# Kernel tuning notes

Hardware: AMD Instinct MI355X
Metric: run time of the kernel (lower is better)

The kernel has to match this reference:

```python
import jax, jax.numpy as jnp
import numpy as np

EPS = 1e-5

def conv2d(x, w, b=None, pad=1):
    # x: [B,C,H,W], w: [O,I,kh,kw]
    y = jax.lax.conv_general_dilated(x, w, (1, 1), [(pad, pad), (pad, pad)],
                                     dimension_numbers=('NCHW', 'OIHW', 'NCHW'))
    if b is not None:
        y = y + b[None, :, None, None]
    return y

def bn(x, g, b, m, v):
    # inference-mode batchnorm
    inv = g / jnp.sqrt(v + EPS)
    return x * inv[None, :, None, None] + (b - m * inv)[None, :, None, None]

def coord_conv(x, w, b):
    B, C, H, W = x.shape
    yy = jnp.broadcast_to(jnp.linspace(-1.0, 1.0, H)[:, None], (H, W))
    xx = jnp.broadcast_to(jnp.linspace(-1.0, 1.0, W)[None, :], (H, W))
    coords = jnp.broadcast_to(jnp.stack([xx, yy])[None], (B, 2, H, W)).astype(x.dtype)
    return conv2d(jnp.concatenate([x, coords], axis=1), w, b, pad=1)

def deform_conv(x, offset, w):
    # deformable conv v1, 3x3, pad=1, stride=1, no bias
    B, C, H, W = x.shape
    K = 9
    # offset channels interleaved (y, x) per kernel tap
    off = offset.reshape(B, K, 2, H, W)
    off_y, off_x = off[:, :, 0], off[:, :, 1]          # [B,9,H,W]
    k = jnp.arange(K)
    ko_y = (k // 3 - 1).astype(x.dtype)[None, :, None, None]
    ko_x = (k % 3 - 1).astype(x.dtype)[None, :, None, None]
    base_y = jnp.arange(H, dtype=x.dtype)[None, None, :, None]
    base_x = jnp.arange(W, dtype=x.dtype)[None, None, None, :]
    py = base_y + ko_y + off_y                          # [B,9,H,W]
    px = base_x + ko_x + off_x
    xf = x.reshape(B, C, H * W)
    y0 = jnp.floor(py)
    x0 = jnp.floor(px)
    acc = jnp.zeros((B, C, K, H, W), x.dtype)
    for dy in (0.0, 1.0):
        for dx in (0.0, 1.0):
            yy = y0 + dy
            xx = x0 + dx
            wgt = (1.0 - jnp.abs(py - yy)) * (1.0 - jnp.abs(px - xx))
            valid = (yy >= 0) & (yy < H) & (xx >= 0) & (xx < W)
            wgt = jnp.where(valid, wgt, 0.0)            # zero padding OOB
            yi = jnp.clip(yy, 0, H - 1).astype(jnp.int32)
            xi = jnp.clip(xx, 0, W - 1).astype(jnp.int32)
            idx = (yi * W + xi).reshape(B, K * H * W)
            v = jnp.take_along_axis(xf, idx[:, None, :], axis=2).reshape(B, C, K, H, W)
            acc = acc + v * wgt[:, None]
    wk = w.reshape(w.shape[0], w.shape[1], K)           # [O,I,9]
    return jnp.einsum('bckhw,ock->bohw', acc, wk)

def setup_inputs() -> dict:
    key = jax.random.key(0)
    ks = jax.random.split(key, 16)
    d_model, hd = 256, 64
    B, H, W = 8, 96, 96
    f32 = jnp.float32
    def bn_params(k):
        k1, k2, k3 = jax.random.split(k, 3)
        return (1.0 + 0.1 * jax.random.normal(k1, (hd,), f32),
                0.1 * jax.random.normal(k2, (hd,), f32),
                0.1 * jax.random.normal(k3, (hd,), f32),
                0.5 + jax.random.uniform(jax.random.fold_in(k, 7), (hd,), f32))
    bn1 = bn_params(ks[1]); bn2 = bn_params(ks[2]); bn3 = bn_params(ks[3]); bn4 = bn_params(ks[4])
    inp = {
        'features': jax.random.normal(ks[0], (B, H, W, d_model), f32),
        'coord_w': 0.05 * jax.random.normal(ks[5], (hd, d_model + 2, 3, 3), f32),
        'coord_b': jnp.zeros((hd,), f32),
        'bn1_g': bn1[0], 'bn1_b': bn1[1], 'bn1_m': bn1[2], 'bn1_v': bn1[3],
        'off_w': 0.01 * jax.random.normal(ks[6], (18, hd, 3, 3), f32),
        'off_b': 0.01 * jax.random.normal(ks[7], (18,), f32),
        'dc_w': 0.05 * jax.random.normal(ks[8], (hd, hd, 3, 3), f32),
        'bn2_g': bn2[0], 'bn2_b': bn2[1], 'bn2_m': bn2[2], 'bn2_v': bn2[3],
        'r1_w': 0.05 * jax.random.normal(ks[9], (hd, hd, 3, 3), f32),
        'bn3_g': bn3[0], 'bn3_b': bn3[1], 'bn3_m': bn3[2], 'bn3_v': bn3[3],
        'r2_w': 0.05 * jax.random.normal(ks[10], (hd, hd, 3, 3), f32),
        'bn4_g': bn4[0], 'bn4_b': bn4[1], 'bn4_m': bn4[2], 'bn4_v': bn4[3],
        'out_w': 0.1 * jax.random.normal(ks[11], (1, hd, 1, 1), f32),
        'out_b': jnp.zeros((1,), f32),
    }
    return inp

def reference(features, coord_w, coord_b, bn1_g, bn1_b, bn1_m, bn1_v,
              off_w, off_b, dc_w, bn2_g, bn2_b, bn2_m, bn2_v,
              r1_w, bn3_g, bn3_b, bn3_m, bn3_v,
              r2_w, bn4_g, bn4_b, bn4_m, bn4_v, out_w, out_b):
    x = jnp.transpose(features, (0, 3, 1, 2))           # NHWC -> NCHW
    x = jax.nn.relu(bn(coord_conv(x, coord_w, coord_b), bn1_g, bn1_b, bn1_m, bn1_v))
    offset = conv2d(x, off_w, off_b, pad=1)
    x = deform_conv(x, offset, dc_w)
    x = jax.nn.relu(bn(x, bn2_g, bn2_b, bn2_m, bn2_v))
    x = jax.nn.relu(bn(conv2d(x, r1_w, None, pad=1), bn3_g, bn3_b, bn3_m, bn3_v))
    x = jax.nn.relu(bn(conv2d(x, r2_w, None, pad=1), bn4_g, bn4_b, bn4_m, bn4_v))
    return jax.nn.sigmoid(conv2d(x, out_w, out_b, pad=0))
```

## Files before the change

kernel.cpp:

```cpp
#include <hip/hip_runtime.h>


typedef unsigned short u16;
typedef unsigned int u32;
typedef __attribute__((ext_vector_type(8)))  short bf16x8;
typedef __attribute__((ext_vector_type(16))) float f32x16;

#define EPSBN 1e-5f

__device__ __forceinline__ u16 f2bf(float f) {
  u32 u = __builtin_bit_cast(u32, f);
  u32 r = u + 0x7FFFu + ((u >> 16) & 1u);
  return (u16)(r >> 16);
}
__device__ __forceinline__ u32 pk2(float a, float b) {
  return (u32)f2bf(a) | ((u32)f2bf(b) << 16);
}
__device__ __forceinline__ float lo2f(u32 w) { return __builtin_bit_cast(float, w << 16); }
__device__ __forceinline__ float hi2f(u32 w) { return __builtin_bit_cast(float, w & 0xFFFF0000u); }

#define N_WCF 147456
#define N_WCC 9216
#define N_WOF 18432
#define N_W64 36864
#define N_ALLW (N_WCF + N_WCC + N_WOF + 3*N_W64)

__global__ __launch_bounds__(256) void prep_kernel(
    const float* __restrict__ coord_w, const float* __restrict__ off_w,
    const float* __restrict__ dc_w, const float* __restrict__ r1_w,
    const float* __restrict__ r2_w,
    u16* __restrict__ wcf, u16* __restrict__ wcc, u16* __restrict__ wof,
    u16* __restrict__ wdf, u16* __restrict__ wr1, u16* __restrict__ wr2)
{
  int i = blockIdx.x * 256 + threadIdx.x;
  if (i >= N_ALLW) return;
  int d = i;
  if (d < N_WCF) {
    int j = d & 7, lane = (d >> 3) & 63, frag = d >> 9;
    int nt = frag & 1, h = (frag >> 1) & 3, tap = (frag >> 3) % 9, cc = (frag >> 3) / 9;
    int ic = cc * 64 + h * 16 + ((lane >> 5) << 3) + j;
    int oc = nt * 32 + (lane & 31);
    wcf[d] = f2bf(coord_w[((size_t)oc * 258 + ic) * 9 + tap]);
    return;
  }
  d -= N_WCF;
  if (d < N_WCC) {
    int j = d & 7, lane = (d >> 3) & 63, frag = d >> 9;
    int nt = frag & 1, tap = frag >> 1;
    int ic = 256 + ((lane >> 5) << 3) + j;
    int oc = nt * 32 + (lane & 31);
    wcc[d] = (ic < 258) ? f2bf(coord_w[((size_t)oc * 258 + ic) * 9 + tap]) : (u16)0;
    return;
  }
  d -= N_WCC;
  if (d < N_WOF) {
    int j = d & 7, lane = (d >> 3) & 63, frag = d >> 9;
    int h = frag & 3, tap = frag >> 2;
    int ic = h * 16 + ((lane >> 5) << 3) + j;
    int oc = lane & 31;
    wof[d] = (oc < 18) ? f2bf(off_w[((size_t)oc * 64 + ic) * 9 + tap]) : (u16)0;
    return;
  }
  d -= N_WOF;
  int seg = d / N_W64;
  int e = d - seg * N_W64;
  int j = e & 7, lane = (e >> 3) & 63, frag = e >> 9;
  int nt = frag & 1, h = (frag >> 1) & 3, tap = frag >> 3;
  int ic = h * 16 + ((lane >> 5) << 3) + j;
  int oc = nt * 32 + (lane & 31);
  const float* src = (seg == 0) ? dc_w : (seg == 1) ? r1_w : r2_w;
  u16* dst = (seg == 0) ? wdf : (seg == 1) ? wr1 : wr2;
  dst[e] = f2bf(src[((size_t)oc * 64 + ic) * 9 + tap]);
}

__global__ __launch_bounds__(512, 2) void coord_conv_kernel(
    const float* __restrict__ feat, const u16* __restrict__ wcf,
    const u16* __restrict__ wcc, const float* __restrict__ cb,
    const float* __restrict__ g, const float* __restrict__ bb,
    const float* __restrict__ m, const float* __restrict__ v,
    u16* __restrict__ x1b)
{
  __shared__ __align__(16) u16 tile[6 * 34 * 72];
  const int t = threadIdx.x;
  const int wv = t >> 6, lane = t & 63;
  const int l31 = lane & 31, l5 = lane >> 5;
  const int rp = wv & 1, ntw = (wv >> 1) & 1, kh = wv >> 2;
  const int x0 = blockIdx.x * 32, y0 = blockIdx.y * 4, b = blockIdx.z;

  f32x16 acc[2] = {};
  float4 pa[4], pb[4];
  bf16x8 wfr[18];

  auto issueF = [&](int cc) {
    #pragma unroll
    for (int r = 0; r < 4; ++r) {
      const int i = t + r * 512;
      const float4 z = {0.f, 0.f, 0.f, 0.f};
      pa[r] = z; pb[r] = z;
      if (i < 1632) {
        const int px = i >> 3, gg = i & 7;
        const int ly = px / 34, lx = px - ly * 34;
        const int gy = y0 + ly - 1, gx = x0 + lx - 1;
        if ((unsigned)gy < 96u && (unsigned)gx < 96u) {
          const float* p = feat + ((size_t)((b * 96 + gy) * 96 + gx)) * 256
                           + cc * 64 + gg * 8;
          pa[r] = *(const float4*)p;
          pb[r] = *(const float4*)(p + 4);
        }
      }
    }
  };
  auto commitF = [&]() {
    #pragma unroll
    for (int r = 0; r < 4; ++r) {
      const int i = t + r * 512;
      if (i < 1632) {
        const int px = i >> 3, gg = i & 7;
        uint4 o;
        o.x = pk2(pa[r].x, pa[r].y); o.y = pk2(pa[r].z, pa[r].w);
        o.z = pk2(pb[r].x, pb[r].y); o.w = pk2(pb[r].z, pb[r].w);
        *(uint4*)(tile + px * 72 + gg * 8) = o;
      }
    }
  };
  auto loadW = [&](int cc) {
    #pragma unroll
    for (int tap = 0; tap < 9; ++tap)
      #pragma unroll
      for (int hh = 0; hh < 2; ++hh) {
        const int h = kh * 2 + hh;
        wfr[tap * 2 + hh] = *(const bf16x8*)(wcf +
            ((size_t)((((cc * 9 + tap) * 4 + h) * 2) + ntw)) * 512 + lane * 8);
      }
  };

  issueF(0);
  loadW(0);
  for (int cc = 0; cc < 4; ++cc) {
    __syncthreads();
    commitF();
    __syncthreads();
    if (cc < 3) issueF(cc + 1);
    #pragma unroll
    for (int tap = 0; tap < 9; ++tap) {
      const int dy = tap / 3, dx = tap - dy * 3;
      #pragma unroll
      for (int hh = 0; hh < 2; ++hh) {
        const bf16x8 bfr = wfr[tap * 2 + hh];
        #pragma unroll
        for (int ai = 0; ai < 2; ++ai) {
          const bf16x8 afr = *(const bf16x8*)(tile +
              ((rp * 2 + ai + dy) * 34 + l31 + dx) * 72
              + (kh * 2 + hh) * 16 + l5 * 8);
          acc[ai] = __builtin_amdgcn_mfma_f32_32x32x16_bf16(afr, bfr, acc[ai],
                                                            0, 0, 0);
        }
      }
    }
    if (cc < 3) loadW(cc + 1);
  }

  bf16x8 wcr[9];
  if (kh == 0) {
    #pragma unroll
    for (int tap = 0; tap < 9; ++tap)
      wcr[tap] = *(const bf16x8*)(wcc + ((size_t)(tap * 2 + ntw)) * 512
                                  + lane * 8);
  }
  __syncthreads();
  for (int i = t; i < 408; i += 512) {
    const int px = i >> 1, gg = i & 1;
    const int ly = px / 34, lx = px - ly * 34;
    const int gy = y0 + ly - 1, gx = x0 + lx - 1;
    uint4 o = {0u, 0u, 0u, 0u};
    if (gg == 0 && (unsigned)gy < 96u && (unsigned)gx < 96u) {
      const float xx = -1.f + (2.f / 95.f) * (float)gx;
      const float yy = -1.f + (2.f / 95.f) * (float)gy;
      o.x = pk2(xx, yy);
    }
    *(uint4*)(tile + (ly * 34 + lx) * 72 + gg * 8) = o;
  }
  __syncthreads();
  if (kh == 0) {
    #pragma unroll
    for (int tap = 0; tap < 9; ++tap) {
      const int dy = tap / 3, dx = tap - dy * 3;
      #pragma unroll
      for (int ai = 0; ai < 2; ++ai) {
        const bf16x8 afr = *(const bf16x8*)(tile +
            ((rp * 2 + ai + dy) * 34 + l31 + dx) * 72 + l5 * 8);
        acc[ai] = __builtin_amdgcn_mfma_f32_32x32x16_bf16(afr, wcr[tap],
                                                          acc[ai], 0, 0, 0);
      }
    }
  }

  float* redk = (float*)tile;
  const int slot = wv & 3;
  #pragma unroll
  for (int ai = 0; ai < 2; ++ai) {
    __syncthreads();
    if (kh == 1) {
      #pragma unroll
      for (int r = 0; r < 16; ++r)
        redk[(r * 4 + slot) * 64 + lane] = acc[ai][r];
    }
    __syncthreads();
    if (kh == 0) {
      #pragma unroll
      for (int r = 0; r < 16; ++r)
        acc[ai][r] += redk[(r * 4 + slot) * 64 + lane];
    }
  }

  if (kh == 0) {
    const int oc = ntw * 32 + l31;
    const float inv = g[oc] * rsqrtf(v[oc] + EPSBN);
    const float sh = bb[oc] - m[oc] * inv + cb[oc] * inv;
    #pragma unroll
    for (int ai = 0; ai < 2; ++ai) {
      const int y = y0 + rp * 2 + ai;
      #pragma unroll
      for (int r = 0; r < 16; ++r) {
        const int xr = (r & 3) + 8 * (r >> 2) + 4 * l5;
        const float val = fmaxf(fmaf(acc[ai][r], inv, sh), 0.f);
        x1b[((size_t)((b * 96 + y) * 96 + x0 + xr)) * 64 + oc] = f2bf(val);
      }
    }
  }
}

template<int NN, int EPI>
__global__ __launch_bounds__(512, 2) void conv64_kernel(
    const u16* __restrict__ xin, const u16* __restrict__ wf,
    const float* __restrict__ bias,
    const float* __restrict__ g, const float* __restrict__ bb,
    const float* __restrict__ m, const float* __restrict__ v,
    const float* __restrict__ ow, const float* __restrict__ ob,
    void* __restrict__ outp)
{
  __shared__ __align__(16) u16 tile[6 * 34 * 72];
  __shared__ float red2[2][128];
  const int t = threadIdx.x;
  const int wv = t >> 6, lane = t & 63;
  const int l31 = lane & 31, l5 = lane >> 5;
  const int rp  = (NN == 2) ? (wv & 1) : 0;
  const int ntw = (NN == 2) ? ((wv >> 1) & 1) : 0;
  const int row = (NN == 2) ? 0 : (wv & 3);
  const int kh  = wv >> 2;
  const int x0 = blockIdx.x * 32, y0 = blockIdx.y * 4, b = blockIdx.z;

  uint4 pf[4];
  #pragma unroll
  for (int r = 0; r < 4; ++r) {
    const int i = t + r * 512;
    const uint4 z = {0u, 0u, 0u, 0u};
    pf[r] = z;
    if (i < 1632) {
      const int px = i >> 3, gg = i & 7;
      const int ly = px / 34, lx = px - ly * 34;
      const int gy = y0 + ly - 1, gx = x0 + lx - 1;
      if ((unsigned)gy < 96u && (unsigned)gx < 96u)
        pf[r] = *(const uint4*)(xin + (((size_t)((b * 96 + gy) * 96 + gx)) << 6)
                                + gg * 8);
    }
  }
  bf16x8 wfr[18];
  #pragma unroll
  for (int tap = 0; tap < 9; ++tap)
    #pragma unroll
    for (int hh = 0; hh < 2; ++hh) {
      const int h = kh * 2 + hh;
      const size_t f = (NN == 2) ? (size_t)((tap * 4 + h) * 2 + ntw)
                                 : (size_t)(tap * 4 + h);
      wfr[tap * 2 + hh] = *(const bf16x8*)(wf + f * 512 + lane * 8);
    }
  #pragma unroll
  for (int r = 0; r < 4; ++r) {
    const int i = t + r * 512;
    if (i < 1632) {
      const int px = i >> 3, gg = i & 7;
      *(uint4*)(tile + px * 72 + gg * 8) = pf[r];
    }
  }
  __syncthreads();

  constexpr int NA = (NN == 2) ? 2 : 1;
  f32x16 acc[NA] = {};
  #pragma unroll
  for (int tap = 0; tap < 9; ++tap) {
    const int dy = tap / 3, dx = tap - dy * 3;
    #pragma unroll
    for (int hh = 0; hh < 2; ++hh) {
      const int h = kh * 2 + hh;
      #pragma unroll
      for (int ai = 0; ai < NA; ++ai) {
        const int rr = (NN == 2) ? (rp * 2 + ai) : row;
        const bf16x8 afr = *(const bf16x8*)(tile +
            ((rr + dy) * 34 + l31 + dx) * 72 + h * 16 + l5 * 8);
        acc[ai] = __builtin_amdgcn_mfma_f32_32x32x16_bf16(afr, wfr[tap * 2 + hh],
                                                          acc[ai], 0, 0, 0);
      }
    }
  }

  float* redk = (float*)tile;
  const int slot = (NN == 2) ? (wv & 3) : row;
  #pragma unroll
  for (int ai = 0; ai < NA; ++ai) {
    __syncthreads();
    if (kh == 1) {
      #pragma unroll
      for (int r = 0; r < 16; ++r)
        redk[(r * 4 + slot) * 64 + lane] = acc[ai][r];
    }
    __syncthreads();
    if (kh == 0) {
      #pragma unroll
      for (int r = 0; r < 16; ++r)
        acc[ai][r] += redk[(r * 4 + slot) * 64 + lane];
    }
  }

  if constexpr (EPI == 0) {
    if (kh == 0) {
      u16* xo = (u16*)outp;
      const int oc = ntw * 32 + l31;
      const float inv = g[oc] * rsqrtf(v[oc] + EPSBN);
      const float sh = bb[oc] - m[oc] * inv;
      #pragma unroll
      for (int ai = 0; ai < NA; ++ai) {
        const int y = y0 + rp * 2 + ai;
        #pragma unroll
        for (int r = 0; r < 16; ++r) {
          const int xr = (r & 3) + 8 * (r >> 2) + 4 * l5;
          const float val = fmaxf(fmaf(acc[ai][r], inv, sh), 0.f);
          xo[((size_t)((b * 96 + y) * 96 + x0 + xr)) * 64 + oc] = f2bf(val);
        }
      }
    }
  } else if constexpr (EPI == 1) {
    if (kh == 0 && l31 < 18) {
      float* fo = (float*)outp;
      const int y = y0 + row;
      const float bs = bias[l31];
      #pragma unroll
      for (int r = 0; r < 16; ++r) {
        const int xr = (r & 3) + 8 * (r >> 2) + 4 * l5;
        fo[((size_t)((b * 96 + y) * 96 + x0 + xr)) * 18 + l31] = acc[0][r] + bs;
      }
    }
  } else {
    if (kh == 0) {
      const int oc = ntw * 32 + l31;
      const float inv = g[oc] * rsqrtf(v[oc] + EPSBN);
      const float sh = bb[oc] - m[oc] * inv;
      const float wo = ow[oc];
      #pragma unroll
      for (int ai = 0; ai < NA; ++ai) {
        float pr[16];
        #pragma unroll
        for (int r = 0; r < 16; ++r) {
          const float val = fmaxf(fmaf(acc[ai][r], inv, sh), 0.f);
          pr[r] = val * wo;
        }
        #pragma unroll
        for (int mask = 1; mask <= 16; mask <<= 1)
          #pragma unroll
          for (int r = 0; r < 16; ++r)
            pr[r] += __shfl_xor(pr[r], mask);
        if (l31 == 0) {
          #pragma unroll
          for (int r = 0; r < 16; ++r) {
            const int xr = (r & 3) + 8 * (r >> 2) + 4 * l5;
            red2[ntw][(rp * 2 + ai) * 32 + xr] = pr[r];
          }
        }
      }
    }
    __syncthreads();
    if (t < 128) {
      float* fo = (float*)outp;
      const int yy = y0 + (t >> 5), xx = x0 + (t & 31);
      const float val = red2[0][t] + red2[1][t] + ob[0];
      fo[(size_t)(b * 96 + yy) * 96 + xx] = 1.f / (1.f + expf(-val));
    }
  }
}

__global__ __launch_bounds__(512, 4) void deform_kernel(
    const u16* __restrict__ x1b, const float* __restrict__ off,
    const u16* __restrict__ wdf,
    const float* __restrict__ g, const float* __restrict__ bb,
    const float* __restrict__ m, const float* __restrict__ v,
    u16* __restrict__ x2b)
{
  __shared__ __align__(16) u16 s[2 * 128 * 72];
  __shared__ float offs[128 * 18];
  const int t = threadIdx.x;
  const int wv = t >> 6, lane = t & 63;
  const int l31 = lane & 31, l5 = lane >> 5;
  const int mt = wv & 3, ntw = wv >> 2;
  const int x0 = blockIdx.x * 16, y0 = blockIdx.y * 8, b = blockIdx.z;

  {
    float po[5];
    #pragma unroll
    for (int r = 0; r < 5; ++r) {
      const int i = t + r * 512;
      po[r] = 0.f;
      if (i < 2304) {
        const int p = i / 18, c = i - p * 18;
        const int gy = y0 + (p >> 4), gx = x0 + (p & 15);
        po[r] = off[((size_t)((b * 96 + gy) * 96 + gx)) * 18 + c];
      }
    }
    #pragma unroll
    for (int r = 0; r < 5; ++r) {
      const int i = t + r * 512;
      if (i < 2304) offs[i] = po[r];
    }
  }
  __syncthreads();

  const int sp = t >> 2, part = t & 3;
  const int sy = y0 + (sp >> 4), sx = x0 + (sp & 15);

  uint4 gbuf[8];
  float w4[4];

  auto prefetch = [&](int k) {
    const float oy = offs[sp * 18 + 2 * k];
    const float ox = offs[sp * 18 + 2 * k + 1];
    const float py = (float)(sy + k / 3 - 1) + oy;
    const float px = (float)(sx + k % 3 - 1) + ox;
    const float yf = floorf(py), xf = floorf(px);
    const float fy = py - yf, fx = px - xf;
    const int yi = (int)yf, xi = (int)xf;
    #pragma unroll
    for (int cor = 0; cor < 4; ++cor) {
      const int cy = yi + (cor >> 1), cx = xi + (cor & 1);
      const uint4 z = {0u, 0u, 0u, 0u};
      gbuf[2 * cor] = z; gbuf[2 * cor + 1] = z;
      const float wy = (cor & 2) ? fy : 1.f - fy;
      const float wx = (cor & 1) ? fx : 1.f - fx;
      w4[cor] = 0.f;
      if ((unsigned)cy < 96u && (unsigned)cx < 96u) {
        w4[cor] = wy * wx;
        const u16* p = x1b + ((size_t)((b * 96 + cy) * 96 + cx)) * 64
                       + part * 16;
        gbuf[2 * cor]     = *(const uint4*)p;
        gbuf[2 * cor + 1] = *(const uint4*)(p + 8);
      }
    }
  };
  auto combine = [&](u16* dst) {
    float val[16];
    #pragma unroll
    for (int j = 0; j < 16; ++j) val[j] = 0.f;
    #pragma unroll
    for (int cor = 0; cor < 4; ++cor) {
      const float wgt = w4[cor];
      const u32 uu[8] = {gbuf[2 * cor].x, gbuf[2 * cor].y,
                         gbuf[2 * cor].z, gbuf[2 * cor].w,
                         gbuf[2 * cor + 1].x, gbuf[2 * cor + 1].y,
                         gbuf[2 * cor + 1].z, gbuf[2 * cor + 1].w};
      #pragma unroll
      for (int u = 0; u < 8; ++u) {
        val[2 * u]     = fmaf(wgt, lo2f(uu[u]), val[2 * u]);
        val[2 * u + 1] = fmaf(wgt, hi2f(uu[u]), val[2 * u + 1]);
      }
    }
    u32 pk[8];
    #pragma unroll
    for (int u = 0; u < 8; ++u) pk[u] = pk2(val[2 * u], val[2 * u + 1]);
    uint4 w0 = {pk[0], pk[1], pk[2], pk[3]};
    uint4 w1 = {pk[4], pk[5], pk[6], pk[7]};
    *(uint4*)(dst + sp * 72 + part * 16) = w0;
    *(uint4*)(dst + sp * 72 + part * 16 + 8) = w1;
  };

  f32x16 acc = {};

  prefetch(0);
  combine(s);
  __syncthreads();

  for (int k = 0; k < 9; ++k) {
    u16* cur = s + (k & 1) * 9216;
    if (k < 8) prefetch(k + 1);
    #pragma unroll
    for (int h = 0; h < 4; ++h) {
      const bf16x8 afr = *(const bf16x8*)(cur + (mt * 32 + l31) * 72
                                          + h * 16 + l5 * 8);
      const bf16x8 bfr = *(const bf16x8*)(wdf +
          ((size_t)((k * 4 + h) * 2 + ntw)) * 512 + lane * 8);
      acc = __builtin_amdgcn_mfma_f32_32x32x16_bf16(afr, bfr, acc, 0, 0, 0);
    }
    if (k < 8) combine(s + ((k + 1) & 1) * 9216);
    __syncthreads();
  }

  const int oc = ntw * 32 + l31;
  const float inv = g[oc] * rsqrtf(v[oc] + EPSBN);
  const float sh = bb[oc] - m[oc] * inv;
  #pragma unroll
  for (int r = 0; r < 16; ++r) {
    const int pxi = mt * 32 + (r & 3) + 8 * (r >> 2) + 4 * l5;
    const int y = y0 + (pxi >> 4), x = x0 + (pxi & 15);
    const float val = fmaxf(fmaf(acc[r], inv, sh), 0.f);
    x2b[((size_t)((b * 96 + y) * 96 + x)) * 64 + oc] = f2bf(val);
  }
}

extern "C" void kernel_launch(void* const* d_in, const int* in_sizes, int n_in,
                              void* d_out, int out_size, void* d_ws,
                              size_t ws_size, hipStream_t stream)
{
  (void)in_sizes; (void)n_in; (void)out_size; (void)ws_size;
  const float* features = (const float*)d_in[0];
  const float* coord_w  = (const float*)d_in[1];
  const float* coord_b  = (const float*)d_in[2];
  const float* bn1g = (const float*)d_in[3];
  const float* bn1b = (const float*)d_in[4];
  const float* bn1m = (const float*)d_in[5];
  const float* bn1v = (const float*)d_in[6];
  const float* off_w = (const float*)d_in[7];
  const float* off_b = (const float*)d_in[8];
  const float* dc_w  = (const float*)d_in[9];
  const float* bn2g = (const float*)d_in[10];
  const float* bn2b = (const float*)d_in[11];
  const float* bn2m = (const float*)d_in[12];
  const float* bn2v = (const float*)d_in[13];
  const float* r1_w = (const float*)d_in[14];
  const float* bn3g = (const float*)d_in[15];
  const float* bn3b = (const float*)d_in[16];
  const float* bn3m = (const float*)d_in[17];
  const float* bn3v = (const float*)d_in[18];
  const float* r2_w = (const float*)d_in[19];
  const float* bn4g = (const float*)d_in[20];
  const float* bn4b = (const float*)d_in[21];
  const float* bn4m = (const float*)d_in[22];
  const float* bn4v = (const float*)d_in[23];
  const float* out_w = (const float*)d_in[24];
  const float* out_b = (const float*)d_in[25];

  char* W = (char*)d_ws;
  float* offb = (float*)W;
  u16*   x1b  = (u16*)(W + 5308416);
  u16*   x2b  = (u16*)(W + 14745600);
  u16*   x3b  = (u16*)(W + 24182784);
  u16*   wcf  = (u16*)(W + 33619968);
  u16*   wcc  = wcf + N_WCF;
  u16*   wof  = wcc + N_WCC;
  u16*   wdf  = wof + N_WOF;
  u16*   wr1  = wdf + N_W64;
  u16*   wr2  = wr1 + N_W64;

  prep_kernel<<<(N_ALLW + 255) / 256, 256, 0, stream>>>(
      coord_w, off_w, dc_w, r1_w, r2_w, wcf, wcc, wof, wdf, wr1, wr2);

  dim3 grid(3, 24, 8);
  dim3 gridD(6, 12, 8);

  coord_conv_kernel<<<grid, 512, 0, stream>>>(
      features, wcf, wcc, coord_b, bn1g, bn1b, bn1m, bn1v, x1b);
  conv64_kernel<1, 1><<<grid, 512, 0, stream>>>(
      x1b, wof, off_b, nullptr, nullptr, nullptr, nullptr, nullptr, nullptr,
      (void*)offb);
  deform_kernel<<<gridD, 512, 0, stream>>>(
      x1b, offb, wdf, bn2g, bn2b, bn2m, bn2v, x2b);
  conv64_kernel<2, 0><<<grid, 512, 0, stream>>>(
      x2b, wr1, nullptr, bn3g, bn3b, bn3m, bn3v, nullptr, nullptr, (void*)x3b);
  conv64_kernel<2, 2><<<grid, 512, 0, stream>>>(
      x3b, wr2, nullptr, bn4g, bn4b, bn4m, bn4v, out_w, out_b, d_out);
}
```

Before: 251.0 us.

## Pre-convert features to bf16 and stage conv tiles via direct global-to-LDS loads

The prep kernel now also converts the NHWC fp32 feature map to bf16 and zeroes a small pad buffer. The conv kernels stage input halos with global_load_lds 16-byte copies, redirecting out-of-bounds pixels to the zero buffer instead of loading through registers. Blocks shrink to 256 threads (4 waves), each wave computing both 32-channel output tiles, with weights read directly from global memory per MFMA rather than preloaded into registers. Coordinate channels get their own small LDS tile. This adds an extra full pass over the features in prep and drops the register-level prefetch overlap in coord_conv.

```diff
diff --git a/kernel.cpp b/kernel.cpp
--- a/kernel.cpp
+++ b/kernel.cpp
@@ -18,6 +18,12 @@
 }
 __device__ __forceinline__ float lo2f(u32 w) { return __builtin_bit_cast(float, w << 16); }
 __device__ __forceinline__ float hi2f(u32 w) { return __builtin_bit_cast(float, w & 0xFFFF0000u); }
+
+__device__ __forceinline__ void gload_lds16(const void* g, void* l) {
+  __builtin_amdgcn_global_load_lds(
+      (const __attribute__((address_space(1))) unsigned int*)g,
+      (__attribute__((address_space(3))) unsigned int*)l, 16, 0, 0);
+}
 
 #define N_WCF 147456
 #define N_WCC 9216
@@ -25,14 +31,32 @@
 #define N_W64 36864
 #define N_ALLW (N_WCF + N_WCC + N_WOF + 3*N_W64)
 
+#define FBK_BLOCKS 9216
+#define WT_BLOCKS  1116
+
 __global__ __launch_bounds__(256) void prep_kernel(
+    const float* __restrict__ feat,
     const float* __restrict__ coord_w, const float* __restrict__ off_w,
     const float* __restrict__ dc_w, const float* __restrict__ r1_w,
     const float* __restrict__ r2_w,
+    u16* __restrict__ fb,
     u16* __restrict__ wcf, u16* __restrict__ wcc, u16* __restrict__ wof,
-    u16* __restrict__ wdf, u16* __restrict__ wr1, u16* __restrict__ wr2)
+    u16* __restrict__ wdf, u16* __restrict__ wr1, u16* __restrict__ wr2,
+    u32* __restrict__ zb)
 {
-  int i = blockIdx.x * 256 + threadIdx.x;
+  const int t = threadIdx.x;
+  if (blockIdx.x < FBK_BLOCKS) {
+    const int e = (blockIdx.x * 256 + t) * 8;
+    const float4 f0 = *(const float4*)(feat + e);
+    const float4 f1 = *(const float4*)(feat + e + 4);
+    uint4 o;
+    o.x = pk2(f0.x, f0.y); o.y = pk2(f0.z, f0.w);
+    o.z = pk2(f1.x, f1.y); o.w = pk2(f1.z, f1.w);
+    *(uint4*)(fb + e) = o;
+    return;
+  }
+  int i = (blockIdx.x - FBK_BLOCKS) * 256 + t;
+  if (i < 64) zb[i] = 0u;
   if (i >= N_ALLW) return;
   int d = i;
   if (d < N_WCF) {
@@ -73,296 +97,262 @@
   dst[e] = f2bf(src[((size_t)oc * 64 + ic) * 9 + tap]);
 }
 
-__global__ __launch_bounds__(512, 2) void coord_conv_kernel(
-    const float* __restrict__ feat, const u16* __restrict__ wcf,
+__device__ __forceinline__ u32 stage_desc(int slot, int x0, int y0, int b,
+                                          int px_stride) {
+  const int px = slot / 9, part = slot - px * 9;
+  if (part >= 8 || px >= 204) return 0xFFFFFFFFu;
+  const int ly = px / 34, lx = px - ly * 34;
+  const int gy = y0 + ly - 1, gx = x0 + lx - 1;
+  if ((unsigned)gy >= 96u || (unsigned)gx >= 96u) return 0xFFFFFFFFu;
+  return (u32)(((b * 96 + gy) * 96 + gx) * px_stride + part * 16);
+}
+
+__global__ __launch_bounds__(256, 4) void coord_conv_kernel(
+    const u16* __restrict__ fb, const u16* __restrict__ wcf,
     const u16* __restrict__ wcc, const float* __restrict__ cb,
     const float* __restrict__ g, const float* __restrict__ bb,
     const float* __restrict__ m, const float* __restrict__ v,
-    u16* __restrict__ x1b)
+    u16* __restrict__ x1b, const u32* __restrict__ zb)
 {
-  __shared__ __align__(16) u16 tile[6 * 34 * 72];
+  __shared__ __align__(16) u16 tile[16384];
+  __shared__ __align__(16) u16 ct[204 * 16];
   const int t = threadIdx.x;
   const int wv = t >> 6, lane = t & 63;
   const int l31 = lane & 31, l5 = lane >> 5;
-  const int rp = wv & 1, ntw = (wv >> 1) & 1, kh = wv >> 2;
+  const int rp = wv & 1, kh = wv >> 1;
   const int x0 = blockIdx.x * 32, y0 = blockIdx.y * 4, b = blockIdx.z;
 
-  f32x16 acc[2] = {};
-  float4 pa[4], pb[4];
-  bf16x8 wfr[18];
-
-  auto issueF = [&](int cc) {
-    #pragma unroll
-    for (int r = 0; r < 4; ++r) {
-      const int i = t + r * 512;
-      const float4 z = {0.f, 0.f, 0.f, 0.f};
-      pa[r] = z; pb[r] = z;
-      if (i < 1632) {
-        const int px = i >> 3, gg = i & 7;
-        const int ly = px / 34, lx = px - ly * 34;
-        const int gy = y0 + ly - 1, gx = x0 + lx - 1;
-        if ((unsigned)gy < 96u && (unsigned)gx < 96u) {
-          const float* p = feat + ((size_t)((b * 96 + gy) * 96 + gx)) * 256
-                           + cc * 64 + gg * 8;
-          pa[r] = *(const float4*)p;
-          pb[r] = *(const float4*)(p + 4);
-        }
-      }
-    }
-  };
-  auto commitF = [&]() {
-    #pragma unroll
-    for (int r = 0; r < 4; ++r) {
-      const int i = t + r * 512;
-      if (i < 1632) {
-        const int px = i >> 3, gg = i & 7;
-        uint4 o;
-        o.x = pk2(pa[r].x, pa[r].y); o.y = pk2(pa[r].z, pa[r].w);
-        o.z = pk2(pb[r].x, pb[r].y); o.w = pk2(pb[r].z, pb[r].w);
-        *(uint4*)(tile + px * 72 + gg * 8) = o;
-      }
-    }
-  };
-  auto loadW = [&](int cc) {
-    #pragma unroll
-    for (int tap = 0; tap < 9; ++tap)
+  u32 desc[8];
+  #pragma unroll
+  for (int k = 0; k < 8; ++k)
+    desc[k] = stage_desc((wv + 4 * k) * 64 + lane, x0, y0, b, 512);
+
+  if (t < 204) {
+    const int ly = t / 34, lx = t - ly * 34;
+    const int gy = y0 + ly - 1, gx = x0 + lx - 1;
+    uint4 o0 = {0u, 0u, 0u, 0u}, o1 = {0u, 0u, 0u, 0u};
+    if ((unsigned)gy < 96u && (unsigned)gx < 96u) {
+      const float xx = -1.f + (2.f / 95.f) * (float)gx;
+      const float yy = -1.f + (2.f / 95.f) * (float)gy;
+      o0.x = pk2(xx, yy);
+    }
+    *(uint4*)(ct + t * 16) = o0;
+    *(uint4*)(ct + t * 16 + 8) = o1;
+  }
+
+  f32x16 acc[2][2] = {};
+
+  for (int cc = 0; cc < 4; ++cc) {
+    #pragma unroll
+    for (int k = 0; k < 8; ++k) {
+      const char* src = (desc[k] == 0xFFFFFFFFu)
+          ? (const char*)zb : (const char*)fb + desc[k] + cc * 128;
+      gload_lds16(src, (char*)tile + (wv + 4 * k) * 1024);
+    }
+    __syncthreads();
+    #pragma unroll
+    for (int tap = 0; tap < 9; ++tap) {
+      const int dy = tap / 3, dx = tap - dy * 3;
       #pragma unroll
       for (int hh = 0; hh < 2; ++hh) {
         const int h = kh * 2 + hh;
-        wfr[tap * 2 + hh] = *(const bf16x8*)(wcf +
-            ((size_t)((((cc * 9 + tap) * 4 + h) * 2) + ntw)) * 512 + lane * 8);
-      }
-  };
-
-  issueF(0);
-  loadW(0);
-  for (int cc = 0; cc < 4; ++cc) {
+        const bf16x8 a0 = *(const bf16x8*)(tile +
+            ((rp * 2 + 0 + dy) * 34 + l31 + dx) * 72 + h * 16 + l5 * 8);
+        const bf16x8 a1 = *(const bf16x8*)(tile +
+            ((rp * 2 + 1 + dy) * 34 + l31 + dx) * 72 + h * 16 + l5 * 8);
+        #pragma unroll
+        for (int nt = 0; nt < 2; ++nt) {
+          const bf16x8 bfr = *(const bf16x8*)(wcf +
+              ((size_t)((((cc * 9 + tap) * 4 + h) * 2) + nt)) * 512 + lane * 8);
+          acc[0][nt] = __builtin_amdgcn_mfma_f32_32x32x16_bf16(a0, bfr,
+                                                               acc[0][nt], 0, 0, 0);
+          acc[1][nt] = __builtin_amdgcn_mfma_f32_32x32x16_bf16(a1, bfr,
+                                                               acc[1][nt], 0, 0, 0);
+        }
+      }
+    }
     __syncthreads();
-    commitF();
-    __syncthreads();
-    if (cc < 3) issueF(cc + 1);
+  }
+
+  if (kh == 0) {
     #pragma unroll
     for (int tap = 0; tap < 9; ++tap) {
       const int dy = tap / 3, dx = tap - dy * 3;
-      #pragma unroll
-      for (int hh = 0; hh < 2; ++hh) {
-        const bf16x8 bfr = wfr[tap * 2 + hh];
-        #pragma unroll
-        for (int ai = 0; ai < 2; ++ai) {
-          const bf16x8 afr = *(const bf16x8*)(tile +
-              ((rp * 2 + ai + dy) * 34 + l31 + dx) * 72
-              + (kh * 2 + hh) * 16 + l5 * 8);
-          acc[ai] = __builtin_amdgcn_mfma_f32_32x32x16_bf16(afr, bfr, acc[ai],
-                                                            0, 0, 0);
+      const bf16x8 a0 = *(const bf16x8*)(ct +
+          ((rp * 2 + 0 + dy) * 34 + l31 + dx) * 16 + l5 * 8);
+      const bf16x8 a1 = *(const bf16x8*)(ct +
+          ((rp * 2 + 1 + dy) * 34 + l31 + dx) * 16 + l5 * 8);
+      #pragma unroll
+      for (int nt = 0; nt < 2; ++nt) {
+        const bf16x8 bfr = *(const bf16x8*)(wcc +
+            ((size_t)(tap * 2 + nt)) * 512 + lane * 8);
+        acc[0][nt] = __builtin_amdgcn_mfma_f32_32x32x16_bf16(a0, bfr,
+                                                             acc[0][nt], 0, 0, 0);
+        acc[1][nt] = __builtin_amdgcn_mfma_f32_32x32x16_bf16(a1, bfr,
+                                                             acc[1][nt], 0, 0, 0);
+      }
+    }
+  }
+
+  float* redk = (float*)tile;
+  __syncthreads();
+  if (kh == 1) {
+    #pragma unroll
+    for (int ai = 0; ai < 2; ++ai)
+      #pragma unroll
+      for (int nt = 0; nt < 2; ++nt)
+        #pragma unroll
+        for (int r = 0; r < 16; ++r)
+          redk[(((rp * 2 + ai) * 2 + nt) * 16 + r) * 64 + lane] = acc[ai][nt][r];
+  }
+  __syncthreads();
+  if (kh == 0) {
+    #pragma unroll
+    for (int ai = 0; ai < 2; ++ai)
+      #pragma unroll
+      for (int nt = 0; nt < 2; ++nt) {
+        #pragma unroll
+        for (int r = 0; r < 16; ++r)
+          acc[ai][nt][r] += redk[(((rp * 2 + ai) * 2 + nt) * 16 + r) * 64 + lane];
+        const int oc = nt * 32 + l31;
+        const float inv = g[oc] * rsqrtf(v[oc] + EPSBN);
+        const float sh = bb[oc] - m[oc] * inv + cb[oc] * inv;
+        const int y = y0 + rp * 2 + ai;
+        #pragma unroll
+        for (int r = 0; r < 16; ++r) {
+          const int xr = (r & 3) + 8 * (r >> 2) + 4 * l5;
+          const float val = fmaxf(fmaf(acc[ai][nt][r], inv, sh), 0.f);
+          x1b[((size_t)((b * 96 + y) * 96 + x0 + xr)) * 64 + oc] = f2bf(val);
         }
       }
-    }
-    if (cc < 3) loadW(cc + 1);
-  }
-
-  bf16x8 wcr[9];
-  if (kh == 0) {
-    #pragma unroll
-    for (int tap = 0; tap < 9; ++tap)
-      wcr[tap] = *(const bf16x8*)(wcc + ((size_t)(tap * 2 + ntw)) * 512
-                                  + lane * 8);
-  }
-  __syncthreads();
-  for (int i = t; i < 408; i += 512) {
-    const int px = i >> 1, gg = i & 1;
-    const int ly = px / 34, lx = px - ly * 34;
-    const int gy = y0 + ly - 1, gx = x0 + lx - 1;
-    uint4 o = {0u, 0u, 0u, 0u};
-    if (gg == 0 && (unsigned)gy < 96u && (unsigned)gx < 96u) {
-      const float xx = -1.f + (2.f / 95.f) * (float)gx;
-      const float yy = -1.f + (2.f / 95.f) * (float)gy;
-      o.x = pk2(xx, yy);
-    }
-    *(uint4*)(tile + (ly * 34 + lx) * 72 + gg * 8) = o;
-  }
-  __syncthreads();
-  if (kh == 0) {
-    #pragma unroll
-    for (int tap = 0; tap < 9; ++tap) {
-      const int dy = tap / 3, dx = tap - dy * 3;
-      #pragma unroll
-      for (int ai = 0; ai < 2; ++ai) {
-        const bf16x8 afr = *(const bf16x8*)(tile +
-            ((rp * 2 + ai + dy) * 34 + l31 + dx) * 72 + l5 * 8);
-        acc[ai] = __builtin_amdgcn_mfma_f32_32x32x16_bf16(afr, wcr[tap],
-                                                          acc[ai], 0, 0, 0);
-      }
-    }
-  }
-
-  float* redk = (float*)tile;
-  const int slot = wv & 3;
-  #pragma unroll
-  for (int ai = 0; ai < 2; ++ai) {
-    __syncthreads();
-    if (kh == 1) {
-      #pragma unroll
-      for (int r = 0; r < 16; ++r)
-        redk[(r * 4 + slot) * 64 + lane] = acc[ai][r];
-    }
-    __syncthreads();
-    if (kh == 0) {
-      #pragma unroll
-      for (int r = 0; r < 16; ++r)
-        acc[ai][r] += redk[(r * 4 + slot) * 64 + lane];
-    }
-  }
-
-  if (kh == 0) {
-    const int oc = ntw * 32 + l31;
-    const float inv = g[oc] * rsqrtf(v[oc] + EPSBN);
-    const float sh = bb[oc] - m[oc] * inv + cb[oc] * inv;
-    #pragma unroll
-    for (int ai = 0; ai < 2; ++ai) {
-      const int y = y0 + rp * 2 + ai;
-      #pragma unroll
-      for (int r = 0; r < 16; ++r) {
-        const int xr = (r & 3) + 8 * (r >> 2) + 4 * l5;
-        const float val = fmaxf(fmaf(acc[ai][r], inv, sh), 0.f);
-        x1b[((size_t)((b * 96 + y) * 96 + x0 + xr)) * 64 + oc] = f2bf(val);
-      }
-    }
   }
 }
 
 template<int NN, int EPI>
-__global__ __launch_bounds__(512, 2) void conv64_kernel(
+__global__ __launch_bounds__(256, 4) void conv64_kernel(
     const u16* __restrict__ xin, const u16* __restrict__ wf,
     const float* __restrict__ bias,
     const float* __restrict__ g, const float* __restrict__ bb,
     const float* __restrict__ m, const float* __restrict__ v,
     const float* __restrict__ ow, const float* __restrict__ ob,
-    void* __restrict__ outp)
+    void* __restrict__ outp, const u32* __restrict__ zb)
 {
-  __shared__ __align__(16) u16 tile[6 * 34 * 72];
-  __shared__ float red2[2][128];
+  __shared__ __align__(16) u16 tile[16384];
+  __shared__ float red2[128];
   const int t = threadIdx.x;
   const int wv = t >> 6, lane = t & 63;
   const int l31 = lane & 31, l5 = lane >> 5;
-  const int rp  = (NN == 2) ? (wv & 1) : 0;
-  const int ntw = (NN == 2) ? ((wv >> 1) & 1) : 0;
-  const int row = (NN == 2) ? 0 : (wv & 3);
-  const int kh  = wv >> 2;
+  const int rp = wv & 1, kh = wv >> 1;
   const int x0 = blockIdx.x * 32, y0 = blockIdx.y * 4, b = blockIdx.z;
 
-  uint4 pf[4];
   #pragma unroll
-  for (int r = 0; r < 4; ++r) {
-    const int i = t + r * 512;
-    const uint4 z = {0u, 0u, 0u, 0u};
-    pf[r] = z;
-    if (i < 1632) {
-      const int px = i >> 3, gg = i & 7;
-      const int ly = px / 34, lx = px - ly * 34;
-      const int gy = y0 + ly - 1, gx = x0 + lx - 1;
-      if ((unsigned)gy < 96u && (unsigned)gx < 96u)
-        pf[r] = *(const uint4*)(xin + (((size_t)((b * 96 + gy) * 96 + gx)) << 6)
-                                + gg * 8);
-    }
-  }
-  bf16x8 wfr[18];
-  #pragma unroll
-  for (int tap = 0; tap < 9; ++tap)
-    #pragma unroll
-    for (int hh = 0; hh < 2; ++hh) {
-      const int h = kh * 2 + hh;
-      const size_t f = (NN == 2) ? (size_t)((tap * 4 + h) * 2 + ntw)
-                                 : (size_t)(tap * 4 + h);
-      wfr[tap * 2 + hh] = *(const bf16x8*)(wf + f * 512 + lane * 8);
-    }
-  #pragma unroll
-  for (int r = 0; r < 4; ++r) {
-    const int i = t + r * 512;
-    if (i < 1632) {
-      const int px = i >> 3, gg = i & 7;
-      *(uint4*)(tile + px * 72 + gg * 8) = pf[r];
-    }
-  }
-  __syncthreads();
-
-  constexpr int NA = (NN == 2) ? 2 : 1;
-  f32x16 acc[NA] = {};
+  for (int k = 0; k < 8; ++k) {
+    const u32 d = stage_desc((wv + 4 * k) * 64 + lane, x0, y0, b, 128);
+    const char* src = (d == 0xFFFFFFFFu) ? (const char*)zb
+                                         : (const char*)xin + d;
+    gload_lds16(src, (char*)tile + (wv + 4 * k) * 1024);
+  }
+  __syncthreads();
+
+  f32x16 acc[2][NN] = {};
   #pragma unroll
   for (int tap = 0; tap < 9; ++tap) {
     const int dy = tap / 3, dx = tap - dy * 3;
     #pragma unroll
     for (int hh = 0; hh < 2; ++hh) {
       const int h = kh * 2 + hh;
-      #pragma unroll
-      for (int ai = 0; ai < NA; ++ai) {
-        const int rr = (NN == 2) ? (rp * 2 + ai) : row;
-        const bf16x8 afr = *(const bf16x8*)(tile +
-            ((rr + dy) * 34 + l31 + dx) * 72 + h * 16 + l5 * 8);
-        acc[ai] = __builtin_amdgcn_mfma_f32_32x32x16_bf16(afr, wfr[tap * 2 + hh],
-                                                          acc[ai], 0, 0, 0);
+      const bf16x8 a0 = *(const bf16x8*)(tile +
+          ((rp * 2 + 0 + dy) * 34 + l31 + dx) * 72 + h * 16 + l5 * 8);
+      const bf16x8 a1 = *(const bf16x8*)(tile +
+          ((rp * 2 + 1 + dy) * 34 + l31 + dx) * 72 + h * 16 + l5 * 8);
+      #pragma unroll
+      for (int nt = 0; nt < NN; ++nt) {
+        const size_t f = (NN == 2) ? (size_t)((tap * 4 + h) * 2 + nt)
+                                   : (size_t)(tap * 4 + h);
+        const bf16x8 bfr = *(const bf16x8*)(wf + f * 512 + lane * 8);
+        acc[0][nt] = __builtin_amdgcn_mfma_f32_32x32x16_bf16(a0, bfr,
+                                                             acc[0][nt], 0, 0, 0);
+        acc[1][nt] = __builtin_amdgcn_mfma_f32_32x32x16_bf16(a1, bfr,
+                                                             acc[1][nt], 0, 0, 0);
       }
     }
   }
 
   float* redk = (float*)tile;
-  const int slot = (NN == 2) ? (wv & 3) : row;
-  #pragma unroll
-  for (int ai = 0; ai < NA; ++ai) {
-    __syncthreads();
-    if (kh == 1) {
-      #pragma unroll
-      for (int r = 0; r < 16; ++r)
-        redk[(r * 4 + slot) * 64 + lane] = acc[ai][r];
-    }
-    __syncthreads();
-    if (kh == 0) {
-      #pragma unroll
-      for (int r = 0; r < 16; ++r)
-        acc[ai][r] += redk[(r * 4 + slot) * 64 + lane];
-    }
-  }
+  __syncthreads();
+  if (kh == 1) {
+    #pragma unroll
+    for (int ai = 0; ai < 2; ++ai)
+      #pragma unroll
+      for (int nt = 0; nt < NN; ++nt)
+        #pragma unroll
+        for (int r = 0; r < 16; ++r)
+          redk[(((rp * 2 + ai) * NN + nt) * 16 + r) * 64 + lane] = acc[ai][nt][r];
+  }
+  __syncthreads();
 
   if constexpr (EPI == 0) {
     if (kh == 0) {
       u16* xo = (u16*)outp;
-      const int oc = ntw * 32 + l31;
-      const float inv = g[oc] * rsqrtf(v[oc] + EPSBN);
-      const float sh = bb[oc] - m[oc] * inv;
-      #pragma unroll
-      for (int ai = 0; ai < NA; ++ai) {
-        const int y = y0 + rp * 2 + ai;
-        #pragma unroll
-        for (int r = 0; r < 16; ++r) {
-          const int xr = (r & 3) + 8 * (r >> 2) + 4 * l5;
-          const float val = fmaxf(fmaf(acc[ai][r], inv, sh), 0.f);
-          xo[((size_t)((b * 96 + y) * 96 + x0 + xr)) * 64 + oc] = f2bf(val);
+      #pragma unroll
+      for (int ai = 0; ai < 2; ++ai)
+        #pragma unroll
+        for (int nt = 0; nt < NN; ++nt) {
+          #pragma unroll
+          for (int r = 0; r < 16; ++r)
+            acc[ai][nt][r] += redk[(((rp * 2 + ai) * NN + nt) * 16 + r) * 64 + lane];
+          const int oc = nt * 32 + l31;
+          const float inv = g[oc] * rsqrtf(v[oc] + EPSBN);
+          const float sh = bb[oc] - m[oc] * inv;
+          const int y = y0 + rp * 2 + ai;
+          #pragma unroll
+          for (int r = 0; r < 16; ++r) {
+            const int xr = (r & 3) + 8 * (r >> 2) + 4 * l5;
+            const float val = fmaxf(fmaf(acc[ai][nt][r], inv, sh), 0.f);
+            xo[((size_t)((b * 96 + y) * 96 + x0 + xr)) * 64 + oc] = f2bf(val);
+          }
         }
-      }
     }
   } else if constexpr (EPI == 1) {
-    if (kh == 0 && l31 < 18) {
+    if (kh == 0) {
       float* fo = (float*)outp;
-      const int y = y0 + row;
-      const float bs = bias[l31];
-      #pragma unroll
-      for (int r = 0; r < 16; ++r) {
-        const int xr = (r & 3) + 8 * (r >> 2) + 4 * l5;
-        fo[((size_t)((b * 96 + y) * 96 + x0 + xr)) * 18 + l31] = acc[0][r] + bs;
+      #pragma unroll
+      for (int ai = 0; ai < 2; ++ai) {
+        #pragma unroll
+        for (int r = 0; r < 16; ++r)
+          acc[ai][0][r] += redk[(((rp * 2 + ai) * NN + 0) * 16 + r) * 64 + lane];
+        if (l31 < 18) {
+          const float bs = bias[l31];
+          const int y = y0 + rp * 2 + ai;
+          #pragma unroll
+          for (int r = 0; r < 16; ++r) {
+            const int xr = (r & 3) + 8 * (r >> 2) + 4 * l5;
+            fo[((size_t)((b * 96 + y) * 96 + x0 + xr)) * 18 + l31] =
+                acc[ai][0][r] + bs;
+          }
+        }
       }
     }
   } else {
     if (kh == 0) {
-      const int oc = ntw * 32 + l31;
-      const float inv = g[oc] * rsqrtf(v[oc] + EPSBN);
-      const float sh = bb[oc] - m[oc] * inv;
-      const float wo = ow[oc];
-      #pragma unroll
-      for (int ai = 0; ai < NA; ++ai) {
+      #pragma unroll
+      for (int ai = 0; ai < 2; ++ai) {
         float pr[16];
         #pragma unroll
-        for (int r = 0; r < 16; ++r) {
-          const float val = fmaxf(fmaf(acc[ai][r], inv, sh), 0.f);
-          pr[r] = val * wo;
+        for (int r = 0; r < 16; ++r) pr[r] = 0.f;
+        #pragma unroll
+        for (int nt = 0; nt < NN; ++nt) {
+          const int oc = nt * 32 + l31;
+          const float inv = g[oc] * rsqrtf(v[oc] + EPSBN);
+          const float sh = bb[oc] - m[oc] * inv;
+          const float wo = ow[oc];
+          #pragma unroll
+          for (int r = 0; r < 16; ++r) {
+            const float a = acc[ai][nt][r] +
+                redk[(((rp * 2 + ai) * NN + nt) * 16 + r) * 64 + lane];
+            const float val = fmaxf(fmaf(a, inv, sh), 0.f);
+            pr[r] = fmaf(val, wo, pr[r]);
+          }
         }
         #pragma unroll
         for (int mask = 1; mask <= 16; mask <<= 1)
@@ -373,7 +363,7 @@
           #pragma unroll
           for (int r = 0; r < 16; ++r) {
             const int xr = (r & 3) + 8 * (r >> 2) + 4 * l5;
-            red2[ntw][(rp * 2 + ai) * 32 + xr] = pr[r];
+            red2[(rp * 2 + ai) * 32 + xr] = pr[r];
           }
         }
       }
@@ -382,7 +372,7 @@
     if (t < 128) {
       float* fo = (float*)outp;
       const int yy = y0 + (t >> 5), xx = x0 + (t & 31);
-      const float val = red2[0][t] + red2[1][t] + ob[0];
+      const float val = red2[t] + ob[0];
       fo[(size_t)(b * 96 + yy) * 96 + xx] = 1.f / (1.f + expf(-val));
     }
   }
@@ -556,22 +546,26 @@
   u16*   wdf  = wof + N_WOF;
   u16*   wr1  = wdf + N_W64;
   u16*   wr2  = wr1 + N_W64;
-
-  prep_kernel<<<(N_ALLW + 255) / 256, 256, 0, stream>>>(
-      coord_w, off_w, dc_w, r1_w, r2_w, wcf, wcc, wof, wdf, wr1, wr2);
+  u16*   fb   = (u16*)(W + 34191360);
+  u32*   zb   = (u32*)(W + 71940096);
+
+  prep_kernel<<<FBK_BLOCKS + WT_BLOCKS, 256, 0, stream>>>(
+      features, coord_w, off_w, dc_w, r1_w, r2_w,
+      fb, wcf, wcc, wof, wdf, wr1, wr2, zb);
 
   dim3 grid(3, 24, 8);
   dim3 gridD(6, 12, 8);
 
-  coord_conv_kernel<<<grid, 512, 0, stream>>>(
-      features, wcf, wcc, coord_b, bn1g, bn1b, bn1m, bn1v, x1b);
-  conv64_kernel<1, 1><<<grid, 512, 0, stream>>>(
+  coord_conv_kernel<<<grid, 256, 0, stream>>>(
+      fb, wcf, wcc, coord_b, bn1g, bn1b, bn1m, bn1v, x1b, zb);
+  conv64_kernel<1, 1><<<grid, 256, 0, stream>>>(
       x1b, wof, off_b, nullptr, nullptr, nullptr, nullptr, nullptr, nullptr,
-      (void*)offb);
+      (void*)offb, zb);
   deform_kernel<<<gridD, 512, 0, stream>>>(
       x1b, offb, wdf, bn2g, bn2b, bn2m, bn2v, x2b);
-  conv64_kernel<2, 0><<<grid, 512, 0, stream>>>(
-      x2b, wr1, nullptr, bn3g, bn3b, bn3m, bn3v, nullptr, nullptr, (void*)x3b);
-  conv64_kernel<2, 2><<<grid, 512, 0, stream>>>(
-      x3b, wr2, nullptr, bn4g, bn4b, bn4m, bn4v, out_w, out_b, d_out);
-}
+  conv64_kernel<2, 0><<<grid, 256, 0, stream>>>(
+      x2b, wr1, nullptr, bn3g, bn3b, bn3m, bn3v, nullptr, nullptr,
+      (void*)x3b, zb);
+  conv64_kernel<2, 2><<<grid, 256, 0, stream>>>(
+      x3b, wr2, nullptr, bn4g, bn4b, bn4m, bn4v, out_w, out_b, d_out, zb);
+}
```

New measurement: 282.1 us. +12.4%, slower.
